# Performance work log

Hardware: AMD Instinct MI355X
Metric: run time of the kernel (lower is better)

Reference implementation:

```python
import jax, jax.numpy as jnp
import numpy as np

N_QUBITS = 10
Q_DEPTH = 6
MAX_LAYERS = 15
DIM = 2 ** N_QUBITS
INV_SQRT2 = 0.7071067811865476

# PennyLane ordering: wire 0 is the most-significant bit of the state index.
# All gates (H, RY, CNOT) are real, so the state stays real float32.

def _split(state, wire):
    a = 2 ** wire
    b = 2 ** (N_QUBITS - wire - 1)
    return state.reshape(-1, a, 2, b)

def apply_h(state, wire):
    s = _split(state, wire)
    s0, s1 = s[:, :, 0], s[:, :, 1]
    out = jnp.stack([(s0 + s1) * INV_SQRT2, (s0 - s1) * INV_SQRT2], axis=2)
    return out.reshape(-1, DIM)

def apply_ry(state, theta, wire):
    # theta: scalar (shared weight) or (B,) per-sample angle
    c = jnp.cos(theta * 0.5).reshape(-1, 1, 1)
    sn = jnp.sin(theta * 0.5).reshape(-1, 1, 1)
    s = _split(state, wire)
    s0, s1 = s[:, :, 0], s[:, :, 1]
    out = jnp.stack([c * s0 - sn * s1, sn * s0 + c * s1], axis=2)
    return out.reshape(-1, DIM)

def apply_cnot(state, ctrl):
    # CNOT on adjacent wires [ctrl, ctrl+1]
    a = 2 ** ctrl
    b = 2 ** (N_QUBITS - ctrl - 2)
    s = state.reshape(-1, a, 2, 2, b)
    out = jnp.stack([s[:, :, 0], s[:, :, 1, ::-1]], axis=2)
    return out.reshape(-1, DIM)

def expval_z(state):
    # <Z_j> = P(qubit j = 0) - P(qubit j = 1)
    zs = []
    for w in range(N_QUBITS):
        s = _split(state, w)
        p = s * s
        zs.append(jnp.sum(p[:, :, 0], axis=(1, 2)) - jnp.sum(p[:, :, 1], axis=(1, 2)))
    return jnp.stack(zs, axis=1)  # (B, n_qubits)

def simulate(q_in, q_params):
    B = q_in.shape[0]
    qw = q_params.reshape(MAX_LAYERS, N_QUBITS)
    state = jnp.zeros((B, DIM), q_in.dtype).at[:, 0].set(1.0)
    for w in range(N_QUBITS):
        state = apply_h(state, w)
    for w in range(N_QUBITS):
        state = apply_ry(state, q_in[:, w], w)
    for k in range(Q_DEPTH):
        for i in range(0, N_QUBITS - 1, 2):
            state = apply_cnot(state, i)
        for i in range(1, N_QUBITS - 1, 2):
            state = apply_cnot(state, i)
        for w in range(N_QUBITS):
            state = apply_ry(state, qw[k + 1, w], w)
    return expval_z(state)

def setup_inputs() -> dict:
    key = jax.random.key(0)
    k1, k2, k3, k4, k5 = jax.random.split(key, 5)
    B, D_IN, N_CLASSES = 8192, 512, 2
    return {
        "input_features": jax.random.normal(k1, (B, D_IN), jnp.float32),
        "W_red": jax.random.normal(k2, (N_QUBITS, D_IN), jnp.float32) * 0.04,
        "b_red": jnp.zeros((N_QUBITS,), jnp.float32),
        "q_params": 0.01 * jax.random.normal(k3, (MAX_LAYERS * N_QUBITS,), jnp.float32),
        "W_post": jax.random.normal(k4, (N_CLASSES, N_QUBITS), jnp.float32) * 0.3,
        "b_post": jax.random.normal(k5, (N_CLASSES,), jnp.float32) * 0.01,
    }

def reference(input_features, W_red, b_red, q_params, W_post, b_post):
    pre_out = input_features @ W_red.T + b_red           # (B, n_qubits)
    q_in = jnp.tanh(pre_out) * (np.pi / 2.0)             # angles in (-pi/2, pi/2)
    q_out = simulate(q_in, q_params)                     # (B, n_qubits) PauliZ expvals
    return q_out @ W_post.T + b_post                     # (B, n_classes)
```

## Files before the change

### kernel.cpp

```cpp
#include <hip/hip_runtime.h>
#include <math.h>

#define QDEPTH 6

typedef _Float16 h2 __attribute__((ext_vector_type(2)));
typedef _Float16 v8h __attribute__((ext_vector_type(8)));
typedef float    v4f __attribute__((ext_vector_type(4)));
typedef unsigned uu4 __attribute__((ext_vector_type(4)));

__device__ __forceinline__ int   h2i(h2 v)  { return __builtin_bit_cast(int, v); }
__device__ __forceinline__ h2    ih2(int v) { return __builtin_bit_cast(h2, v); }
__device__ __forceinline__ unsigned h2u(h2 v) { return __builtin_bit_cast(unsigned, v); }

__device__ __forceinline__ h2 bper(int addr, h2 v) {
  return ih2(__builtin_amdgcn_ds_bpermute(addr, h2i(v)));
}

template<int CTRL>
__device__ __forceinline__ h2 dpph(h2 v) {
  int i = h2i(v);
  return ih2(__builtin_amdgcn_update_dpp(i, i, CTRL, 0xF, 0xF, true));
}

template<int CTRL>
__device__ __forceinline__ float dpp_add0(float v) {
  int i = __float_as_int(v);
  int r = __builtin_amdgcn_update_dpp(0, i, CTRL, 0xF, 0xF, false);
  return v + __int_as_float(r);
}

__device__ __forceinline__ float wave_sum(float v) {
  v = dpp_add0<0x111>(v);
  v = dpp_add0<0x112>(v);
  v = dpp_add0<0x114>(v);
  v = dpp_add0<0x118>(v);
  v = dpp_add0<0x142>(v);
  v = dpp_add0<0x143>(v);
  return v;
}

__device__ __forceinline__ float bcast63(float v) {
  return __int_as_float(__builtin_amdgcn_readlane(__float_as_int(v), 63));
}

__device__ __forceinline__ void pl32s(int& a, int& b) {
  asm("v_permlane32_swap_b32 %0, %1" : "+v"(a), "+v"(b));
}
__device__ __forceinline__ void pl16s(int& a, int& b) {
  asm("v_permlane16_swap_b32 %0, %1" : "+v"(a), "+v"(b));
}

__device__ __forceinline__ void apply_layers(h2 (&x)[8], const unsigned* sco,
                                             int lane, int addrP, int addrX4,
                                             bool cb1) {
  for (int k = 0; k < QDEPTH; ++k) {
    const unsigned* L = sco + k * 29;
#pragma unroll
    for (int i = 0; i < 8; ++i) x[i] = bper(addrP, x[i]);
    { h2 t = x[4]; x[4] = x[6]; x[6] = t; t = x[5]; x[5] = x[7]; x[7] = t; }
    { h2 t = x[2]; x[2] = x[3]; x[3] = t; t = x[6]; x[6] = x[7]; x[7] = t; }
    { h2 cc9 = ih2(L[27]), ms9 = ih2(L[28]);
#pragma unroll
      for (int i = 0; i < 8; ++i) {
        h2 t = __builtin_shufflevector(x[i], x[i], 1, 0);
        bool flg = (i == 1 || i == 2 || i == 5 || i == 6);
        x[i] = flg ? (h2)(t * cc9 + x[i] * ms9) : (h2)(x[i] * cc9 + t * ms9);
      } }
    { h2 cc6 = ih2(L[18]), ss6 = ih2(L[19]), ns6 = ih2(L[20]);
      h2 AA = cb1 ? ns6 : cc6;
      h2 BB = cb1 ? cc6 : ns6;
      h2 CC = cb1 ? cc6 : ss6;
      h2 DD = cb1 ? ss6 : cc6;
#pragma unroll
      for (int i = 0; i < 4; ++i) {
        h2 u = x[i], w = x[i + 4];
        x[i]     = u * AA + w * BB;
        x[i + 4] = u * CC + w * DD;
      } }
    { h2 cc7 = ih2(L[21]), ss7 = ih2(L[22]), ns7 = ih2(L[23]);
#pragma unroll
      for (int i = 0; i < 8; ++i) if (!(i & 2)) {
        h2 u = x[i], w = x[i | 2];
        x[i]     = u * cc7 + w * ns7;
        x[i | 2] = w * cc7 + u * ss7;
      } }
    { h2 cc8 = ih2(L[24]), ss8 = ih2(L[25]), ns8 = ih2(L[26]);
#pragma unroll
      for (int i = 0; i < 8; ++i) if (!(i & 1)) {
        h2 u = x[i], w = x[i | 1];
        x[i]     = u * cc8 + w * ns8;
        x[i | 1] = w * cc8 + u * ss8;
      } }
    { h2 cc0 = ih2(L[0]), ss0 = ih2(L[1]), ns0 = ih2(L[2]);
#pragma unroll
      for (int j = 0; j < 4; ++j) {
        int a = h2i(x[2 * j]), b = h2i(x[2 * j + 1]);
        pl32s(a, b);
        h2 u = ih2(a), v = ih2(b);
        h2 nu = u * cc0 + v * ns0;
        h2 nv = v * cc0 + u * ss0;
        int na = h2i(nu), nb = h2i(nv);
        pl32s(na, nb);
        x[2 * j] = ih2(na); x[2 * j + 1] = ih2(nb);
      } }
    { h2 cc1 = ih2(L[3]), ss1 = ih2(L[4]), ns1 = ih2(L[5]);
#pragma unroll
      for (int j = 0; j < 4; ++j) {
        int a = h2i(x[2 * j]), b = h2i(x[2 * j + 1]);
        pl16s(a, b);
        h2 u = ih2(a), v = ih2(b);
        h2 nu = u * cc1 + v * ns1;
        h2 nv = v * cc1 + u * ss1;
        int na = h2i(nu), nb = h2i(nv);
        pl16s(na, nb);
        x[2 * j] = ih2(na); x[2 * j + 1] = ih2(nb);
      } }
    { h2 cc2 = ih2(L[6]), ss2 = ih2(L[7]), ns2 = ih2(L[8]);
      h2 gg = (lane & 8) ? ss2 : ns2;
#pragma unroll
      for (int i = 0; i < 8; ++i) {
        h2 p = dpph<0x128>(x[i]);
        x[i] = x[i] * cc2 + p * gg;
      } }
    { h2 cc3 = ih2(L[9]), ss3 = ih2(L[10]), ns3 = ih2(L[11]);
      h2 gg = (lane & 4) ? ss3 : ns3;
#pragma unroll
      for (int i = 0; i < 8; ++i) {
        h2 p = bper(addrX4, x[i]);
        x[i] = x[i] * cc3 + p * gg;
      } }
    { h2 cc4 = ih2(L[12]), ss4 = ih2(L[13]), ns4 = ih2(L[14]);
      h2 gg = (lane & 2) ? ss4 : ns4;
#pragma unroll
      for (int i = 0; i < 8; ++i) {
        h2 p = dpph<0x4E>(x[i]);
        x[i] = x[i] * cc4 + p * gg;
      } }
    { h2 cc5 = ih2(L[15]), ss5 = ih2(L[16]), ns5 = ih2(L[17]);
      h2 gg = (lane & 1) ? ss5 : ns5;
#pragma unroll
      for (int i = 0; i < 8; ++i) {
        h2 p = dpph<0xB1>(x[i]);
        x[i] = x[i] * cc5 + p * gg;
      } }
  }
}

__device__ __forceinline__ void fill_sco(const float* qp, unsigned* sco) {
  int t = threadIdx.x;
  if (t < 60) {
    int k = t / 10, w = t % 10;
    float ang = qp[(k + 1) * 10 + w] * 0.5f;
    float c = __cosf(ang), s = __sinf(ang);
    _Float16 ch = (_Float16)c, sh = (_Float16)s, nh = (_Float16)(-s);
    if (w < 9) {
      sco[k * 29 + w * 3 + 0] = h2u((h2){ch, ch});
      sco[k * 29 + w * 3 + 1] = h2u((h2){sh, sh});
      sco[k * 29 + w * 3 + 2] = h2u((h2){nh, nh});
    } else {
      sco[k * 29 + 27] = h2u((h2){ch, ch});
      sco[k * 29 + 28] = h2u((h2){nh, sh});
    }
  }
}

__global__ void __launch_bounds__(256) prep_kernel(
    const float* __restrict__ qp, const float* __restrict__ Wpost,
    const float* __restrict__ inp, const float* __restrict__ Wred,
    const float* __restrict__ bred, const float* __restrict__ bpost,
    unsigned short* __restrict__ Bswz,
    unsigned short* __restrict__ glaneP,
    unsigned short* __restrict__ greg,
    float* __restrict__ w0, float* __restrict__ w1,
    float* __restrict__ out) {
  int lane = threadIdx.x & 63;

  if (blockIdx.x < 256) {
    __shared__ unsigned sco[QDEPTH * 29];
    fill_sco(qp, sco);
    __syncthreads();

    int i = blockIdx.x * 4 + (threadIdx.x >> 6);

    if (blockIdx.x == 0) {
      for (int n = threadIdx.x; n < 1024; n += 256) {
        float a0 = 0.f, a1 = 0.f;
#pragma unroll
        for (int w = 0; w < 10; ++w) {
          float sg = ((n >> (9 - w)) & 1) ? -1.f : 1.f;
          a0 += sg * Wpost[w];
          a1 += sg * Wpost[10 + w];
        }
        w0[n] = a0; w1[n] = a1;
      }
    }

    int o = lane ^ (((lane >> 4) & 1) << 3) ^ (((lane >> 2) & 1) << 1);
    int psrc = o ^ (((o >> 5) & 1) << 4) ^ (((o >> 3) & 1) << 2) ^ ((o >> 1) & 1);
    int addrP = psrc << 2, addrX4 = (lane ^ 4) << 2;
    bool cb1 = lane & 1;

    h2 x[8];
#pragma unroll
    for (int r = 0; r < 8; ++r) {
      int base = lane * 16 + 2 * r;
      x[r] = (h2){ (_Float16)(base == i ? 1.f : 0.f),
                   (_Float16)(base + 1 == i ? 1.f : 0.f) };
    }
    apply_layers(x, sco, lane, addrP, addrX4, cb1);

    int kt = i >> 5, kk = i & 31;
    int jj = kk & 7, hi16 = (kk >> 3) << 4;
    size_t tbase = ((size_t)(lane * 32 + kt)) << 9;
#pragma unroll
    for (int r = 0; r < 8; ++r) {
      unsigned u = h2u(x[r]);
      Bswz[tbase + (size_t)((hi16 | (2 * r)) * 8 + jj)]     = (unsigned short)(u & 0xFFFF);
      Bswz[tbase + (size_t)((hi16 | (2 * r + 1)) * 8 + jj)] = (unsigned short)(u >> 16);
    }
  } else {
    int wv = (blockIdx.x - 256) * 4 + (threadIdx.x >> 6);

    const float4* rA = (const float4*)(inp + (size_t)(2 * wv) * 512);
    const float4* rB = (const float4*)(inp + (size_t)(2 * wv + 1) * 512);
    float4 A0 = rA[lane], A1 = rA[lane + 64];
    float4 B0 = rB[lane], B1 = rB[lane + 64];
    float thA[10], thB[10];
#pragma unroll
    for (int q = 0; q < 10; ++q) {
      const float4* w4 = (const float4*)(Wred + q * 512);
      float4 w0v = w4[lane], w1v = w4[lane + 64];
      thA[q] = A0.x * w0v.x + A0.y * w0v.y + A0.z * w0v.z + A0.w * w0v.w
             + A1.x * w1v.x + A1.y * w1v.y + A1.z * w1v.z + A1.w * w1v.w;
      thB[q] = B0.x * w0v.x + B0.y * w0v.y + B0.z * w0v.z + B0.w * w0v.w
             + B1.x * w1v.x + B1.y * w1v.y + B1.z * w1v.z + B1.w * w1v.w;
    }

#pragma unroll
    for (int e = 0; e < 2; ++e) {
      int el = 2 * wv + e;
      float g0[10], g1[10];
#pragma unroll
      for (int q = 0; q < 10; ++q) {
        float tot = bcast63(wave_sum(e ? thB[q] : thA[q])) + bred[q];
        float xc = fminf(fmaxf(tot, -15.f), 15.f);
        float u = __expf(2.f * xc);
        float tanhv = (u - 1.f) * __builtin_amdgcn_rcpf(u + 1.f);
        float t = tanhv * 0.78539816339744831f;
        float c = __cosf(t), s = __sinf(t);
        g0[q] = (c - s) * 0.70710678118654752f;
        g1[q] = (c + s) * 0.70710678118654752f;
      }
      float lf = 1.f;
#pragma unroll
      for (int w = 0; w < 6; ++w)
        lf *= ((lane >> (5 - w)) & 1) ? g1[w] : g0[w];
      glaneP[((size_t)(lane & 1) * 8192 + el) * 32 + (lane >> 1)] =
          (unsigned short)(h2u((h2){(_Float16)lf, (_Float16)lf}) & 0xFFFF);
      if (lane < 16) {
        int t4 = lane;
        float gg = ((t4 & 8) ? g1[6] : g0[6]) * ((t4 & 4) ? g1[7] : g0[7])
                 * ((t4 & 2) ? g1[8] : g0[8]) * ((t4 & 1) ? g1[9] : g0[9]);
        greg[(size_t)el * 16 + t4] =
            (unsigned short)(h2u((h2){(_Float16)gg, (_Float16)gg}) & 0xFFFF);
      }
      if (lane == 0) {
        out[2 * (size_t)el]     = bpost[0];
        out[2 * (size_t)el + 1] = bpost[1];
      }
    }
  }
}

__global__ void __launch_bounds__(256, 4) gemm_kernel(
    const unsigned short* __restrict__ Bswz,
    const unsigned short* __restrict__ glaneP,
    const unsigned short* __restrict__ greg,
    const float* __restrict__ w0, const float* __restrict__ w1,
    float* __restrict__ out) {
  int bm = blockIdx.x >> 4, bn = blockIdx.x & 15;
  int wvL  = threadIdx.x >> 6;
  int lane = threadIdx.x & 63;
  int wm = wvL >> 1, wn = wvL & 1;
  int l15 = lane & 15, lhi = lane >> 4;
  int gsel = lhi >> 1;
  int hh   = lhi & 1;
  int rowBase = bm * 128 + wm * 64;
  int ntG0 = bn * 4 + wn * 2;

  int eA[4];
  h2 grf[4][4];
  const uu4* glp[4];
#pragma unroll
  for (int mt = 0; mt < 4; ++mt) {
    eA[mt] = rowBase + mt * 16 + l15;
    const uu4* gp = (const uu4*)(greg + (size_t)eA[mt] * 16 + hh * 8);
    uu4 gu = *gp;
    grf[mt][0] = ih2(gu.x); grf[mt][1] = ih2(gu.y);
    grf[mt][2] = ih2(gu.z); grf[mt][3] = ih2(gu.w);
    glp[mt] = (const uu4*)(glaneP + ((size_t)gsel * 8192 + eA[mt]) * 32);
  }

  v4f acc[4][2];
#pragma unroll
  for (int mt = 0; mt < 4; ++mt) {
    acc[mt][0] = (v4f){0.f, 0.f, 0.f, 0.f};
    acc[mt][1] = (v4f){0.f, 0.f, 0.f, 0.f};
  }

#pragma unroll 1
  for (int c = 0; c < 4; ++c) {
    uu4 gu[4];
#pragma unroll
    for (int mt = 0; mt < 4; ++mt) gu[mt] = glp[mt][c];
#pragma unroll
    for (int t = 0; t < 8; ++t) {
      int kt = c * 8 + t;
      v8h bf0, bf1;
      {
        const uu4* bp0 = (const uu4*)(Bswz + (((size_t)(ntG0)     * 32 + kt) << 9)) + lane;
        const uu4* bp1 = (const uu4*)(Bswz + (((size_t)(ntG0 + 1) * 32 + kt) << 9)) + lane;
        bf0 = __builtin_bit_cast(v8h, *bp0);
        bf1 = __builtin_bit_cast(v8h, *bp1);
      }
      unsigned sel = (t & 1) ? 0x03020302u : 0x01000100u;
#pragma unroll
      for (int mt = 0; mt < 4; ++mt) {
        unsigned word = gu[mt][t >> 1];
        h2 g2 = ih2((int)__builtin_amdgcn_perm(word, word, sel));
        uu4 au;
        au.x = h2u(g2 * grf[mt][0]);
        au.y = h2u(g2 * grf[mt][1]);
        au.z = h2u(g2 * grf[mt][2]);
        au.w = h2u(g2 * grf[mt][3]);
        v8h af = __builtin_bit_cast(v8h, au);
        acc[mt][0] = __builtin_amdgcn_mfma_f32_16x16x32_f16(af, bf0, acc[mt][0], 0, 0, 0);
        acc[mt][1] = __builtin_amdgcn_mfma_f32_16x16x32_f16(af, bf1, acc[mt][1], 0, 0, 0);
      }
    }
  }

  float wa[2], wb[2];
#pragma unroll
  for (int nt = 0; nt < 2; ++nt) {
    int n = bn * 64 + wn * 32 + nt * 16 + l15;
    wa[nt] = w0[n]; wb[nt] = w1[n];
  }
#pragma unroll
  for (int mt = 0; mt < 4; ++mt) {
#pragma unroll
    for (int j = 0; j < 4; ++j) {
      float c0 = acc[mt][0][j], c1 = acc[mt][1][j];
      float p0 = c0 * c0 * wa[0] + c1 * c1 * wa[1];
      float p1 = c0 * c0 * wb[0] + c1 * c1 * wb[1];
      p0 += __shfl_xor(p0, 1, 64); p1 += __shfl_xor(p1, 1, 64);
      p0 += __shfl_xor(p0, 2, 64); p1 += __shfl_xor(p1, 2, 64);
      p0 += __shfl_xor(p0, 4, 64); p1 += __shfl_xor(p1, 4, 64);
      p0 += __shfl_xor(p0, 8, 64); p1 += __shfl_xor(p1, 8, 64);
      if (l15 == 0) {
        int e = rowBase + mt * 16 + lhi * 4 + j;
        atomicAdd(&out[2 * (size_t)e],     p0);
        atomicAdd(&out[2 * (size_t)e + 1], p1);
      }
    }
  }
}

extern "C" void kernel_launch(void* const* d_in, const int* in_sizes, int n_in,
                              void* d_out, int out_size, void* d_ws, size_t ws_size,
                              hipStream_t stream) {
  const float* inp   = (const float*)d_in[0];
  const float* Wred  = (const float*)d_in[1];
  const float* bred  = (const float*)d_in[2];
  const float* qp    = (const float*)d_in[3];
  const float* Wpost = (const float*)d_in[4];
  const float* bpost = (const float*)d_in[5];
  float* out = (float*)d_out;

  unsigned short* Bswz   = (unsigned short*)d_ws;
  unsigned short* glaneP = (unsigned short*)((char*)d_ws + (2u << 20));
  unsigned short* greg   = (unsigned short*)((char*)d_ws + (3u << 20));
  float* w0 = (float*)((char*)d_ws + (3u << 20) + (256u << 10));
  float* w1 = w0 + 1024;

  int B = in_sizes[0] / 512;

  prep_kernel<<<256 + (B * 32) / 256, 256, 0, stream>>>(
      qp, Wpost, inp, Wred, bred, bpost, Bswz, glaneP, greg, w0, w1, out);
  gemm_kernel<<<(B / 128) * 16, 256, 0, stream>>>(Bswz, glaneP, greg, w0, w1, out);
}
```

Measured before the change: 123.0 us.

## Batch four basis columns per wave in prep and prefetch GEMM operands

```diff
diff --git a/kernel.cpp b/kernel.cpp
--- a/kernel.cpp
+++ b/kernel.cpp
@@ -50,99 +50,128 @@
   asm("v_permlane16_swap_b32 %0, %1" : "+v"(a), "+v"(b));
 }
 
-__device__ __forceinline__ void apply_layers(h2 (&x)[8], const unsigned* sco,
+template<int NB>
+__device__ __forceinline__ void apply_layers(h2 (&x)[NB][8], const unsigned* sco,
                                              int lane, int addrP, int addrX4,
                                              bool cb1) {
   for (int k = 0; k < QDEPTH; ++k) {
     const unsigned* L = sco + k * 29;
 #pragma unroll
-    for (int i = 0; i < 8; ++i) x[i] = bper(addrP, x[i]);
-    { h2 t = x[4]; x[4] = x[6]; x[6] = t; t = x[5]; x[5] = x[7]; x[7] = t; }
-    { h2 t = x[2]; x[2] = x[3]; x[3] = t; t = x[6]; x[6] = x[7]; x[7] = t; }
+    for (int b = 0; b < NB; ++b)
+#pragma unroll
+      for (int i = 0; i < 8; ++i) x[b][i] = bper(addrP, x[b][i]);
+#pragma unroll
+    for (int b = 0; b < NB; ++b) {
+      h2 t = x[b][4]; x[b][4] = x[b][6]; x[b][6] = t;
+      t = x[b][5]; x[b][5] = x[b][7]; x[b][7] = t;
+      t = x[b][2]; x[b][2] = x[b][3]; x[b][3] = t;
+      t = x[b][6]; x[b][6] = x[b][7]; x[b][7] = t;
+    }
     { h2 cc9 = ih2(L[27]), ms9 = ih2(L[28]);
 #pragma unroll
-      for (int i = 0; i < 8; ++i) {
-        h2 t = __builtin_shufflevector(x[i], x[i], 1, 0);
-        bool flg = (i == 1 || i == 2 || i == 5 || i == 6);
-        x[i] = flg ? (h2)(t * cc9 + x[i] * ms9) : (h2)(x[i] * cc9 + t * ms9);
-      } }
+      for (int b = 0; b < NB; ++b)
+#pragma unroll
+        for (int i = 0; i < 8; ++i) {
+          h2 t = __builtin_shufflevector(x[b][i], x[b][i], 1, 0);
+          bool flg = (i == 1 || i == 2 || i == 5 || i == 6);
+          x[b][i] = flg ? (h2)(t * cc9 + x[b][i] * ms9)
+                        : (h2)(x[b][i] * cc9 + t * ms9);
+        } }
     { h2 cc6 = ih2(L[18]), ss6 = ih2(L[19]), ns6 = ih2(L[20]);
       h2 AA = cb1 ? ns6 : cc6;
       h2 BB = cb1 ? cc6 : ns6;
       h2 CC = cb1 ? cc6 : ss6;
       h2 DD = cb1 ? ss6 : cc6;
 #pragma unroll
-      for (int i = 0; i < 4; ++i) {
-        h2 u = x[i], w = x[i + 4];
-        x[i]     = u * AA + w * BB;
-        x[i + 4] = u * CC + w * DD;
-      } }
+      for (int b = 0; b < NB; ++b)
+#pragma unroll
+        for (int i = 0; i < 4; ++i) {
+          h2 u = x[b][i], w = x[b][i + 4];
+          x[b][i]     = u * AA + w * BB;
+          x[b][i + 4] = u * CC + w * DD;
+        } }
     { h2 cc7 = ih2(L[21]), ss7 = ih2(L[22]), ns7 = ih2(L[23]);
 #pragma unroll
-      for (int i = 0; i < 8; ++i) if (!(i & 2)) {
-        h2 u = x[i], w = x[i | 2];
-        x[i]     = u * cc7 + w * ns7;
-        x[i | 2] = w * cc7 + u * ss7;
-      } }
+      for (int b = 0; b < NB; ++b)
+#pragma unroll
+        for (int i = 0; i < 8; ++i) if (!(i & 2)) {
+          h2 u = x[b][i], w = x[b][i | 2];
+          x[b][i]     = u * cc7 + w * ns7;
+          x[b][i | 2] = w * cc7 + u * ss7;
+        } }
     { h2 cc8 = ih2(L[24]), ss8 = ih2(L[25]), ns8 = ih2(L[26]);
 #pragma unroll
-      for (int i = 0; i < 8; ++i) if (!(i & 1)) {
-        h2 u = x[i], w = x[i | 1];
-        x[i]     = u * cc8 + w * ns8;
-        x[i | 1] = w * cc8 + u * ss8;
-      } }
+      for (int b = 0; b < NB; ++b)
+#pragma unroll
+        for (int i = 0; i < 8; ++i) if (!(i & 1)) {
+          h2 u = x[b][i], w = x[b][i | 1];
+          x[b][i]     = u * cc8 + w * ns8;
+          x[b][i | 1] = w * cc8 + u * ss8;
+        } }
     { h2 cc0 = ih2(L[0]), ss0 = ih2(L[1]), ns0 = ih2(L[2]);
 #pragma unroll
-      for (int j = 0; j < 4; ++j) {
-        int a = h2i(x[2 * j]), b = h2i(x[2 * j + 1]);
-        pl32s(a, b);
-        h2 u = ih2(a), v = ih2(b);
-        h2 nu = u * cc0 + v * ns0;
-        h2 nv = v * cc0 + u * ss0;
-        int na = h2i(nu), nb = h2i(nv);
-        pl32s(na, nb);
-        x[2 * j] = ih2(na); x[2 * j + 1] = ih2(nb);
-      } }
+      for (int b = 0; b < NB; ++b)
+#pragma unroll
+        for (int j = 0; j < 4; ++j) {
+          int a = h2i(x[b][2 * j]), bb = h2i(x[b][2 * j + 1]);
+          pl32s(a, bb);
+          h2 u = ih2(a), v = ih2(bb);
+          h2 nu = u * cc0 + v * ns0;
+          h2 nv = v * cc0 + u * ss0;
+          int na = h2i(nu), nb = h2i(nv);
+          pl32s(na, nb);
+          x[b][2 * j] = ih2(na); x[b][2 * j + 1] = ih2(nb);
+        } }
     { h2 cc1 = ih2(L[3]), ss1 = ih2(L[4]), ns1 = ih2(L[5]);
 #pragma unroll
-      for (int j = 0; j < 4; ++j) {
-        int a = h2i(x[2 * j]), b = h2i(x[2 * j + 1]);
-        pl16s(a, b);
-        h2 u = ih2(a), v = ih2(b);
-        h2 nu = u * cc1 + v * ns1;
-        h2 nv = v * cc1 + u * ss1;
-        int na = h2i(nu), nb = h2i(nv);
-        pl16s(na, nb);
-        x[2 * j] = ih2(na); x[2 * j + 1] = ih2(nb);
-      } }
+      for (int b = 0; b < NB; ++b)
+#pragma unroll
+        for (int j = 0; j < 4; ++j) {
+          int a = h2i(x[b][2 * j]), bb = h2i(x[b][2 * j + 1]);
+          pl16s(a, bb);
+          h2 u = ih2(a), v = ih2(bb);
+          h2 nu = u * cc1 + v * ns1;
+          h2 nv = v * cc1 + u * ss1;
+          int na = h2i(nu), nb = h2i(nv);
+          pl16s(na, nb);
+          x[b][2 * j] = ih2(na); x[b][2 * j + 1] = ih2(nb);
+        } }
     { h2 cc2 = ih2(L[6]), ss2 = ih2(L[7]), ns2 = ih2(L[8]);
       h2 gg = (lane & 8) ? ss2 : ns2;
 #pragma unroll
-      for (int i = 0; i < 8; ++i) {
-        h2 p = dpph<0x128>(x[i]);
-        x[i] = x[i] * cc2 + p * gg;
-      } }
+      for (int b = 0; b < NB; ++b)
+#pragma unroll
+        for (int i = 0; i < 8; ++i) {
+          h2 p = dpph<0x128>(x[b][i]);
+          x[b][i] = x[b][i] * cc2 + p * gg;
+        } }
     { h2 cc3 = ih2(L[9]), ss3 = ih2(L[10]), ns3 = ih2(L[11]);
       h2 gg = (lane & 4) ? ss3 : ns3;
 #pragma unroll
-      for (int i = 0; i < 8; ++i) {
-        h2 p = bper(addrX4, x[i]);
-        x[i] = x[i] * cc3 + p * gg;
-      } }
+      for (int b = 0; b < NB; ++b)
+#pragma unroll
+        for (int i = 0; i < 8; ++i) {
+          h2 p = bper(addrX4, x[b][i]);
+          x[b][i] = x[b][i] * cc3 + p * gg;
+        } }
     { h2 cc4 = ih2(L[12]), ss4 = ih2(L[13]), ns4 = ih2(L[14]);
       h2 gg = (lane & 2) ? ss4 : ns4;
 #pragma unroll
-      for (int i = 0; i < 8; ++i) {
-        h2 p = dpph<0x4E>(x[i]);
-        x[i] = x[i] * cc4 + p * gg;
-      } }
+      for (int b = 0; b < NB; ++b)
+#pragma unroll
+        for (int i = 0; i < 8; ++i) {
+          h2 p = dpph<0x4E>(x[b][i]);
+          x[b][i] = x[b][i] * cc4 + p * gg;
+        } }
     { h2 cc5 = ih2(L[15]), ss5 = ih2(L[16]), ns5 = ih2(L[17]);
       h2 gg = (lane & 1) ? ss5 : ns5;
 #pragma unroll
-      for (int i = 0; i < 8; ++i) {
-        h2 p = dpph<0xB1>(x[i]);
-        x[i] = x[i] * cc5 + p * gg;
-      } }
+      for (int b = 0; b < NB; ++b)
+#pragma unroll
+        for (int i = 0; i < 8; ++i) {
+          h2 p = dpph<0xB1>(x[b][i]);
+          x[b][i] = x[b][i] * cc5 + p * gg;
+        } }
   }
 }
 
@@ -175,12 +204,13 @@
     float* __restrict__ out) {
   int lane = threadIdx.x & 63;
 
-  if (blockIdx.x < 256) {
+  if (blockIdx.x < 64) {
     __shared__ unsigned sco[QDEPTH * 29];
     fill_sco(qp, sco);
     __syncthreads();
 
-    int i = blockIdx.x * 4 + (threadIdx.x >> 6);
+    int gw = blockIdx.x * 4 + (threadIdx.x >> 6);
+    int i0 = gw * 4;
 
     if (blockIdx.x == 0) {
       for (int n = threadIdx.x; n < 1024; n += 256) {
@@ -200,26 +230,32 @@
     int addrP = psrc << 2, addrX4 = (lane ^ 4) << 2;
     bool cb1 = lane & 1;
 
-    h2 x[8];
-#pragma unroll
-    for (int r = 0; r < 8; ++r) {
-      int base = lane * 16 + 2 * r;
-      x[r] = (h2){ (_Float16)(base == i ? 1.f : 0.f),
-                   (_Float16)(base + 1 == i ? 1.f : 0.f) };
-    }
-    apply_layers(x, sco, lane, addrP, addrX4, cb1);
-
-    int kt = i >> 5, kk = i & 31;
-    int jj = kk & 7, hi16 = (kk >> 3) << 4;
-    size_t tbase = ((size_t)(lane * 32 + kt)) << 9;
-#pragma unroll
-    for (int r = 0; r < 8; ++r) {
-      unsigned u = h2u(x[r]);
-      Bswz[tbase + (size_t)((hi16 | (2 * r)) * 8 + jj)]     = (unsigned short)(u & 0xFFFF);
-      Bswz[tbase + (size_t)((hi16 | (2 * r + 1)) * 8 + jj)] = (unsigned short)(u >> 16);
+    h2 x[4][8];
+#pragma unroll
+    for (int b = 0; b < 4; ++b)
+#pragma unroll
+      for (int r = 0; r < 8; ++r) {
+        int base = lane * 16 + 2 * r;
+        x[b][r] = (h2){ (_Float16)(base == i0 + b ? 1.f : 0.f),
+                        (_Float16)(base + 1 == i0 + b ? 1.f : 0.f) };
+      }
+    apply_layers<4>(x, sco, lane, addrP, addrX4, cb1);
+
+#pragma unroll
+    for (int b = 0; b < 4; ++b) {
+      int i = i0 + b;
+      int kt = i >> 5, kk = i & 31;
+      int jj = kk & 7, hi16 = (kk >> 3) << 4;
+      size_t tbase = ((size_t)(lane * 32 + kt)) << 9;
+#pragma unroll
+      for (int r = 0; r < 8; ++r) {
+        unsigned u = h2u(x[b][r]);
+        Bswz[tbase + (size_t)((hi16 | (2 * r)) * 8 + jj)]     = (unsigned short)(u & 0xFFFF);
+        Bswz[tbase + (size_t)((hi16 | (2 * r + 1)) * 8 + jj)] = (unsigned short)(u >> 16);
+      }
     }
   } else {
-    int wv = (blockIdx.x - 256) * 4 + (threadIdx.x >> 6);
+    int wv = (blockIdx.x - 64) * 4 + (threadIdx.x >> 6);
 
     const float4* rA = (const float4*)(inp + (size_t)(2 * wv) * 512);
     const float4* rB = (const float4*)(inp + (size_t)(2 * wv + 1) * 512);
@@ -295,9 +331,9 @@
   for (int mt = 0; mt < 4; ++mt) {
     eA[mt] = rowBase + mt * 16 + l15;
     const uu4* gp = (const uu4*)(greg + (size_t)eA[mt] * 16 + hh * 8);
-    uu4 gu = *gp;
-    grf[mt][0] = ih2(gu.x); grf[mt][1] = ih2(gu.y);
-    grf[mt][2] = ih2(gu.z); grf[mt][3] = ih2(gu.w);
+    uu4 gu0 = *gp;
+    grf[mt][0] = ih2(gu0.x); grf[mt][1] = ih2(gu0.y);
+    grf[mt][2] = ih2(gu0.z); grf[mt][3] = ih2(gu0.w);
     glp[mt] = (const uu4*)(glaneP + ((size_t)gsel * 8192 + eA[mt]) * 32);
   }
 
@@ -308,21 +344,29 @@
     acc[mt][1] = (v4f){0.f, 0.f, 0.f, 0.f};
   }
 
+  const uu4* bp0 = (const uu4*)(Bswz + ((size_t)ntG0       * 32 << 9)) + lane;
+  const uu4* bp1 = (const uu4*)(Bswz + ((size_t)(ntG0 + 1) * 32 << 9)) + lane;
+
+  uu4 gu[4], gun[4];
+#pragma unroll
+  for (int mt = 0; mt < 4; ++mt) gu[mt] = glp[mt][0];
+  uu4 bn0 = *bp0, bn1 = *bp1;
+
 #pragma unroll 1
   for (int c = 0; c < 4; ++c) {
-    uu4 gu[4];
-#pragma unroll
-    for (int mt = 0; mt < 4; ++mt) gu[mt] = glp[mt][c];
+    if (c < 3) {
+#pragma unroll
+      for (int mt = 0; mt < 4; ++mt) gun[mt] = glp[mt][c + 1];
+    }
 #pragma unroll
     for (int t = 0; t < 8; ++t) {
-      int kt = c * 8 + t;
-      v8h bf0, bf1;
-      {
-        const uu4* bp0 = (const uu4*)(Bswz + (((size_t)(ntG0)     * 32 + kt) << 9)) + lane;
-        const uu4* bp1 = (const uu4*)(Bswz + (((size_t)(ntG0 + 1) * 32 + kt) << 9)) + lane;
-        bf0 = __builtin_bit_cast(v8h, *bp0);
-        bf1 = __builtin_bit_cast(v8h, *bp1);
-      }
+      uu4 bc0 = bn0, bc1 = bn1;
+      if (c * 8 + t < 31) {
+        bp0 += 64; bp1 += 64;
+        bn0 = *bp0; bn1 = *bp1;
+      }
+      v8h bf0 = __builtin_bit_cast(v8h, bc0);
+      v8h bf1 = __builtin_bit_cast(v8h, bc1);
       unsigned sel = (t & 1) ? 0x03020302u : 0x01000100u;
 #pragma unroll
       for (int mt = 0; mt < 4; ++mt) {
@@ -338,6 +382,8 @@
         acc[mt][1] = __builtin_amdgcn_mfma_f32_16x16x32_f16(af, bf1, acc[mt][1], 0, 0, 0);
       }
     }
+#pragma unroll
+    for (int mt = 0; mt < 4; ++mt) gu[mt] = gun[mt];
   }
 
   float wa[2], wb[2];
@@ -385,7 +431,7 @@
 
   int B = in_sizes[0] / 512;
 
-  prep_kernel<<<256 + (B * 32) / 256, 256, 0, stream>>>(
+  prep_kernel<<<64 + (B * 32) / 256, 256, 0, stream>>>(
       qp, Wpost, inp, Wred, bred, bpost, Bswz, glaneP, greg, w0, w1, out);
   gemm_kernel<<<(B / 128) * 16, 256, 0, stream>>>(Bswz, glaneP, greg, w0, w1, out);
 }
```

New measurement: 125.1 us. About the same (+1.7%).
